# Performance work log

Hardware: AMD Instinct MI355X
Metric: run time of the kernel (lower is better)

Reference implementation:

```python
import jax, jax.numpy as jnp
import numpy as np

N = 12288   # nodes
E = 393216  # edges (avg degree 32)
B = 16      # graphs in batch
F_IN = 15   # node feature dim
H = 32      # hidden_dim
EMB = 64    # embedding_dim
NC = 11     # num_classes
EDIM = 2    # edge feature dim
EPS = 1e-5  # BatchNorm eps


def _bn(x, gamma, beta):
    # training-mode BatchNorm1d: biased batch variance, matches torch normalization
    mu = jnp.mean(x, axis=0)
    var = jnp.var(x, axis=0)
    return gamma * (x - mu) * jax.lax.rsqrt(var + EPS) + beta


def setup_inputs() -> dict:
    key = jax.random.key(0)
    ks = jax.random.split(key, 16)
    def p(k, shape, s=0.05):
        return jax.random.normal(k, shape, dtype=jnp.float32) * s
    z = lambda *s: jnp.zeros(s, jnp.float32)
    o = lambda *s: jnp.ones(s, jnp.float32)
    return {
        "x": jax.random.normal(ks[0], (N, F_IN), dtype=jnp.float32),
        "edge_attr": jax.random.normal(ks[1], (E, EDIM), dtype=jnp.float32),
        "w_edge": p(ks[2], (EDIM, 1)), "b_edge": z(1),
        "w1": p(ks[3], (F_IN, H)), "b1": z(H), "g1": o(H), "be1": z(H),
        "w2": p(ks[4], (H, 2 * H)), "b2": z(2 * H), "g2": o(2 * H), "be2": z(2 * H),
        "w3": p(ks[5], (2 * H, EMB)), "b3": z(EMB), "g3": o(EMB), "be3": z(EMB),
        "wf1": p(ks[6], (EMB, 512)), "bf1": z(512), "gf1": o(512), "bef1": z(512),
        "wf2": p(ks[7], (512, 256)), "bf2": z(256), "gf2": o(256), "bef2": z(256),
        "wf3": p(ks[8], (256, NC)), "bf3": z(NC),
        "edge_index": jax.random.randint(ks[9], (2, E), 0, N, dtype=jnp.int64)
                      if jax.config.jax_enable_x64 else jax.random.randint(ks[9], (2, E), 0, N),
        "batch": jnp.sort(jax.random.randint(ks[10], (N,), 0, B)),
    }


def reference(x, edge_attr, w_edge, b_edge,
              w1, b1, g1, be1, w2, b2, g2, be2, w3, b3, g3, be3,
              wf1, bf1, gf1, bef1, wf2, bf2, gf2, bef2, wf3, bf3,
              edge_index, batch):
    # edge weights: sigmoid(Linear(edge_attr)) -> [E]
    ew = jax.nn.sigmoid(edge_attr @ w_edge + b_edge)[:, 0]
    # dense adjacency with self loops, accumulate duplicates (sparse_coo.to_dense)
    loop = jnp.arange(N)
    row = jnp.concatenate([edge_index[0], loop])
    col = jnp.concatenate([edge_index[1], loop])
    w_aug = jnp.concatenate([ew, jnp.ones((N,), ew.dtype)])
    adj = jnp.zeros((N, N), ew.dtype).at[row, col].add(w_aug)
    # symmetric degree normalization D^-1/2 A D^-1/2
    deg = adj.sum(axis=1)
    dis = jnp.where(deg > 0, jax.lax.rsqrt(jnp.where(deg > 0, deg, 1.0)), 0.0)
    support = dis[:, None] * adj * dis[None, :]
    # three GCN layers: support @ x @ W + b, BN, relu
    h = jax.nn.relu(_bn(support @ x @ w1 + b1, g1, be1))
    h = jax.nn.relu(_bn(support @ h @ w2 + b2, g2, be2))
    h = jax.nn.relu(_bn(support @ h @ w3 + b3, g3, be3))
    # global max pool per graph (empty graphs -> zeros)
    seg = jax.ops.segment_max(h, batch, num_segments=B)
    cnt = jax.ops.segment_sum(jnp.ones((N,), h.dtype), batch, num_segments=B)
    emb = jnp.where(cnt[:, None] > 0, seg, 0.0)
    # MLP head (dropout = identity at inference)
    o = jax.nn.relu(_bn(emb @ wf1 + bf1, gf1, bef1))
    o = jax.nn.relu(_bn(o @ wf2 + bf2, gf2, bef2))
    logits = o @ wf3 + bf3
    return jax.nn.log_softmax(logits, axis=1), emb
```

## Files before the change

### kernel.cpp

```cpp
#include <hip/hip_runtime.h>

#define NN   12288
#define EE   393216
#define WELL 128
#define NELL (NN*WELL)
#define BG   16
#define FIN  15
#define FH1  32
#define FH2  64
#define NCL  11
#define BNEPS 1e-5f
#define NBANK 32

typedef unsigned long long u64;
static inline int cdiv(long a, long b){ return (int)((a + b - 1) / b); }

__device__ __forceinline__ int getIdx(const void* p, long i, int is64){
  return is64 ? (int)((const long long*)p)[i] : ((const int*)p)[i];
}

__device__ __forceinline__ float degOf(unsigned lo){
  return 1.0f + (float)lo * (1.0f/1048576.0f);
}

__global__ void k_pre(u64* deg_cnt, float* csp1, float* csp2, float* csp3,
                      float* embf, float* xp, const float* x,
                      const void* ei, const void* batch, int* flags){
  int g = blockIdx.x*256 + threadIdx.x;
  if (g < NN){
    deg_cnt[g] = 0ull;
    float v[16];
    #pragma unroll
    for (int j = 0; j < 15; j++) v[j] = x[g*15 + j];
    v[15] = 0.f;
    float4* dst = (float4*)(xp + g*16);
    dst[0] = make_float4(v[0],  v[1],  v[2],  v[3]);
    dst[1] = make_float4(v[4],  v[5],  v[6],  v[7]);
    dst[2] = make_float4(v[8],  v[9],  v[10], v[11]);
    dst[3] = make_float4(v[12], v[13], v[14], v[15]);
  }
  if (g < NBANK*128){ csp1[g] = 0.f; csp2[g] = 0.f; csp3[g] = 0.f; }
  if (g < BG*64) embf[g] = 0.f;
  if (blockIdx.x == 0 && threadIdx.x < 64){
    const int* a = (const int*)ei;
    unsigned long long m0 = __ballot(a[2*threadIdx.x + 1] == 0);
    const int* b = (const int*)batch;
    int j = 96*threadIdx.x;
    unsigned long long m1 = __ballot(b[2*j + 1] == 0);
    if (threadIdx.x == 0){
      flags[0] = (m0 == ~0ull) ? 1 : 0;
      flags[1] = (m1 == ~0ull) ? 1 : 0;
    }
  }
}

__global__ void k_edge(const float* ea, const float* we, const float* bedg,
                       const void* ei, const int* flags, u64* deg_cnt,
                       unsigned* csr_p){
  int e = blockIdx.x*256 + threadIdx.x;
  if (e >= EE) return;
  int is64 = flags[0];
  float2 eav = ((const float2*)ea)[e];
  float z = eav.x*we[0] + eav.y*we[1] + bedg[0];
  float w = 1.0f/(1.0f + expf(-z));
  int r = getIdx(ei, e, is64);
  int c = getIdx(ei, (long)EE + e, is64);
  u64 add = (1ull << 32) | (u64)__float2uint_rn(w * 1048576.0f);
  u64 old = atomicAdd(&deg_cnt[r], add);
  int slot = (int)(old >> 32);
  if (slot < WELL){
    unsigned wfix = __float2uint_rn(w * 131072.0f);
    csr_p[((long)r << 7) + slot] = (unsigned)c | (wfix << 14);
  }
}

__global__ void __launch_bounds__(256) k_fix2(const u64* __restrict__ deg_cnt,
                                              unsigned* __restrict__ csr_p){
  int row = blockIdx.x*4 + (threadIdx.x >> 6);
  int lane = threadIdx.x & 63;
  const unsigned* cl = (const unsigned*)deg_cnt;
  int n = (int)(deg_cnt[row] >> 32);
  n = n < WELL ? n : WELL;
  for (int s = lane; s < n; s += 64){
    long idx = ((long)row << 7) + s;
    unsigned v = csr_p[idx];
    int c = (int)(v & 16383u);
    float w = (float)(v >> 14) * (1.0f/131072.0f);
    w *= rsqrtf(degOf(cl[2*c]));
    csr_p[idx] = (unsigned)c | (__float2uint_rn(w * 131072.0f) << 14);
  }
}

template<int F, int FUSE, int LPR, int KS, int FO, int APPLY_BN>
__global__ void __launch_bounds__(256) k_layerv(
    const float* __restrict__ Hin,
    const float* __restrict__ cspin, const float* __restrict__ gam,
    const float* __restrict__ bet,
    const float* __restrict__ W, const float* __restrict__ bias,
    const u64* __restrict__ deg_cnt, const unsigned* __restrict__ csr_p,
    float* __restrict__ Pout, float* __restrict__ csout){
  const int R = 256/(LPR*KS);
  __shared__ __align__(16) float At[R][F];
  __shared__ float4 Apart[256];
  __shared__ float lcs[FO], lcq[FO];
  __shared__ float lsc[64], lsh[64];
  int tid = threadIdx.x;
  if (tid < FO){ lcs[tid] = 0.f; lcq[tid] = 0.f; }
  if (APPLY_BN && tid < F){
    float s = 0.f, q = 0.f;
    #pragma unroll
    for (int b = 0; b < NBANK; b++){
      s += cspin[b*128 + tid];
      q += cspin[b*128 + 64 + tid];
    }
    float mu  = s*(1.0f/NN);
    float var = q*(1.0f/NN) - mu*mu;
    float sc = gam[tid]*rsqrtf(var + BNEPS);
    lsc[tid] = sc;
    lsh[tid] = bet[tid] - mu*sc;
  }
  __syncthreads();
  int fl = tid % LPR;
  int sub = tid / LPR;
  int kw = sub % KS, lr = sub / KS;
  int f0 = fl*4;
  float sc0 = 1.f, sc1 = 1.f, sc2 = 1.f, sc3 = 1.f;
  float sh0 = 0.f, sh1 = 0.f, sh2 = 0.f, sh3 = 0.f;
  if (APPLY_BN){
    sc0 = lsc[f0]; sc1 = lsc[f0+1]; sc2 = lsc[f0+2]; sc3 = lsc[f0+3];
    sh0 = lsh[f0]; sh1 = lsh[f0+1]; sh2 = lsh[f0+2]; sh3 = lsh[f0+3];
  }
  int row = blockIdx.x*R + lr;
  u64 dc = deg_cnt[row];
  float d = rsqrtf(degOf((unsigned)(dc & 0xffffffffull)));
  int n = (int)(dc >> 32);
  n = n < WELL ? n : WELL;
  const float4* __restrict__ Hin4 = (const float4*)Hin;
  float ax = 0.f, ay = 0.f, az = 0.f, aw = 0.f;
  if (kw == 0){
    float4 v = Hin4[row*LPR + fl];
    if (APPLY_BN){
      ax = d * fmaxf(v.x*sc0 + sh0, 0.f);
      ay = d * fmaxf(v.y*sc1 + sh1, 0.f);
      az = d * fmaxf(v.z*sc2 + sh2, 0.f);
      aw = d * fmaxf(v.w*sc3 + sh3, 0.f);
    } else {
      ax = d*v.x; ay = d*v.y; az = d*v.z; aw = d*v.w;
    }
  }
  int nch = (n + 7) >> 3;
  const uint4* pb = (const uint4*)(csr_p + ((long)row << 7));
  int ch = kw;
  if (ch < nch){
    uint4 q0 = pb[2*ch], q1 = pb[2*ch+1];
    while (true){
      int chn = ch + KS;
      bool more = (chn < nch);
      uint4 p0, p1;
      if (more){ p0 = pb[2*chn]; p1 = pb[2*chn+1]; }
      unsigned pv[8];
      pv[0]=q0.x; pv[1]=q0.y; pv[2]=q0.z; pv[3]=q0.w;
      pv[4]=q1.x; pv[5]=q1.y; pv[6]=q1.z; pv[7]=q1.w;
      int base = ch*8;
      if (base + 8 > n){
        #pragma unroll
        for (int j = 0; j < 8; j++) if (base + j >= n) pv[j] = 0u;
      }
      float4 h4[8];
      #pragma unroll
      for (int j = 0; j < 8; j++)
        h4[j] = Hin4[(int)(pv[j] & 16383u)*LPR + fl];
      #pragma unroll
      for (int j = 0; j < 8; j++){
        float w = (float)(pv[j] >> 14) * (1.0f/131072.0f);
        float hx = h4[j].x, hy = h4[j].y, hz = h4[j].z, hw = h4[j].w;
        if (APPLY_BN){
          hx = fmaxf(hx*sc0 + sh0, 0.f);
          hy = fmaxf(hy*sc1 + sh1, 0.f);
          hz = fmaxf(hz*sc2 + sh2, 0.f);
          hw = fmaxf(hw*sc3 + sh3, 0.f);
        }
        ax += w*hx; ay += w*hy; az += w*hz; aw += w*hw;
      }
      if (!more) break;
      ch = chn; q0 = p0; q1 = p1;
    }
  }
  Apart[tid] = make_float4(ax, ay, az, aw);
  __syncthreads();
  if (kw == 0){
    #pragma unroll
    for (int k = 1; k < KS; k++){
      float4 p = Apart[tid + k*LPR];
      ax += p.x; ay += p.y; az += p.z; aw += p.w;
    }
    float4* atrow = (float4*)&At[lr][0];
    atrow[fl] = make_float4(d*ax, d*ay, d*az, d*aw);
  }
  __syncthreads();
  const int fo = tid % FO;
  float bb = bias[fo];
  for (int o = tid; o < R*FO; o += 256){
    int l = o / FO;
    float s = bb;
    const float4* at4 = (const float4*)&At[l][0];
    #pragma unroll
    for (int fi4 = 0; fi4 < FUSE/4; fi4++){
      float4 a = at4[fi4];
      s += a.x * W[(fi4*4 + 0)*FO + fo];
      s += a.y * W[(fi4*4 + 1)*FO + fo];
      s += a.z * W[(fi4*4 + 2)*FO + fo];
      s += a.w * W[(fi4*4 + 3)*FO + fo];
    }
    #pragma unroll
    for (int fi = (FUSE/4)*4; fi < FUSE; fi++)
      s += At[l][fi] * W[fi*FO + fo];
    Pout[(blockIdx.x*R + l)*FO + fo] = s;
    atomicAdd(&lcs[fo], s);
    atomicAdd(&lcq[fo], s*s);
  }
  __syncthreads();
  if (tid < FO){
    int bank = blockIdx.x & (NBANK-1);
    atomicAdd(&csout[bank*128 + tid],      lcs[tid]);
    atomicAdd(&csout[bank*128 + 64 + tid], lcq[tid]);
  }
}

__global__ void k_pool(const float* P3, const float* csp, const float* gam,
                       const float* bet, const void* batch, const int* flags,
                       float* embf){
  __shared__ float lsc[64], lsh[64];
  if (threadIdx.x < 64){
    float s = 0.f, q = 0.f;
    #pragma unroll
    for (int b = 0; b < NBANK; b++){
      s += csp[b*128 + threadIdx.x];
      q += csp[b*128 + 64 + threadIdx.x];
    }
    float mu  = s*(1.0f/NN);
    float var = q*(1.0f/NN) - mu*mu;
    float sc = gam[threadIdx.x]*rsqrtf(var + BNEPS);
    lsc[threadIdx.x] = sc;
    lsh[threadIdx.x] = bet[threadIdx.x] - mu*sc;
  }
  __syncthreads();
  int is64 = flags[1];
  int b = blockIdx.x & 15, chunk = blockIdx.x >> 4;
  int lo = 0, hi = NN;
  while (lo < hi){ int m = (lo+hi)>>1; if (getIdx(batch, m, is64) < b) lo = m+1; else hi = m; }
  int start = lo;
  lo = start; hi = NN;
  while (lo < hi){ int m = (lo+hi)>>1; if (getIdx(batch, m, is64) < b+1) lo = m+1; else hi = m; }
  int end = lo;
  int f = threadIdx.x & 63, grp = threadIdx.x >> 6;
  float sc = lsc[f], sh = lsh[f];
  float m = 0.0f;
  for (int i = start + chunk*4 + grp; i < end; i += 64)
    m = fmaxf(m, P3[(long)i*FH2 + f]*sc + sh);
  __shared__ float shm[4][64];
  shm[grp][f] = m;
  __syncthreads();
  if (grp == 0){
    float v = fmaxf(fmaxf(shm[0][f], shm[1][f]), fmaxf(shm[2][f], shm[3][f]));
    atomicMax((int*)&embf[b*64 + f], __float_as_int(v));
  }
}

__global__ void __launch_bounds__(256) k_fcA(const float* embf, const float* wf1,
    const float* bf1, const float* gf1, const float* bef1, float* s1g, float* out){
  if (blockIdx.x == 0){
    #pragma unroll
    for (int i = 0; i < 4; i++)
      out[BG*NCL + i*256 + threadIdx.x] = embf[i*256 + threadIdx.x];
  }
  int c = blockIdx.x*4 + (threadIdx.x >> 6);
  int l = threadIdx.x & 63;
  float wcol = wf1[l*512 + c];
  float z[BG];
  #pragma unroll
  for (int r = 0; r < BG; r++){
    float v = embf[r*64 + l] * wcol;
    #pragma unroll
    for (int off = 32; off > 0; off >>= 1) v += __shfl_down(v, off);
    z[r] = v;
  }
  if (l == 0){
    float bb = bf1[c];
    float s = 0.f, q = 0.f;
    #pragma unroll
    for (int r = 0; r < BG; r++){ float zr = z[r] + bb; s += zr; q += zr*zr; }
    float mean = s*(1.f/BG), var = q*(1.f/BG) - mean*mean;
    float inv = rsqrtf(var + BNEPS);
    float gg = gf1[c], b2 = bef1[c];
    #pragma unroll
    for (int r = 0; r < BG; r++)
      s1g[r*512 + c] = fmaxf(gg*(z[r] + bb - mean)*inv + b2, 0.f);
  }
}

__global__ void __launch_bounds__(256) k_fcB(const float* s1g, const float* wf2,
    const float* bf2, const float* gf2, const float* bef2, float* s2g){
  int c = blockIdx.x*4 + (threadIdx.x >> 6);
  int l = threadIdx.x & 63;
  float wreg[8];
  #pragma unroll
  for (int j = 0; j < 8; j++) wreg[j] = wf2[(l + 64*j)*256 + c];
  float z[BG];
  #pragma unroll
  for (int r = 0; r < BG; r++){
    float v = 0.f;
    #pragma unroll
    for (int j = 0; j < 8; j++) v += s1g[r*512 + l + 64*j] * wreg[j];
    #pragma unroll
    for (int off = 32; off > 0; off >>= 1) v += __shfl_down(v, off);
    z[r] = v;
  }
  if (l == 0){
    float bb = bf2[c];
    float s = 0.f, q = 0.f;
    #pragma unroll
    for (int r = 0; r < BG; r++){ float zr = z[r] + bb; s += zr; q += zr*zr; }
    float mean = s*(1.f/BG), var = q*(1.f/BG) - mean*mean;
    float inv = rsqrtf(var + BNEPS);
    float gg = gf2[c], b2 = bef2[c];
    #pragma unroll
    for (int r = 0; r < BG; r++)
      s2g[r*256 + c] = fmaxf(gg*(z[r] + bb - mean)*inv + b2, 0.f);
  }
}

__global__ void k_fc3(const float* s2g, const float* wf3, const float* bf3, float* out){
  __shared__ float s2[BG*256];
  __shared__ float sl[BG*NCL];
  int t = threadIdx.x;
  for (int i = t; i < BG*256; i += 256) s2[i] = s2g[i];
  __syncthreads();
  if (t < BG*NCL){
    int r = t / NCL, c = t - r*NCL;
    float s = bf3[c];
    for (int k = 0; k < 256; k++) s += s2[r*256 + k]*wf3[k*NCL + c];
    sl[t] = s;
  }
  __syncthreads();
  if (t < BG){
    float m = -1e30f;
    for (int c = 0; c < NCL; c++) m = fmaxf(m, sl[t*NCL + c]);
    float s = 0.f;
    for (int c = 0; c < NCL; c++) s += expf(sl[t*NCL + c] - m);
    float lg = logf(s) + m;
    for (int c = 0; c < NCL; c++) out[t*NCL + c] = sl[t*NCL + c] - lg;
  }
}

extern "C" void kernel_launch(void* const* d_in, const int* in_sizes, int n_in,
                              void* d_out, int out_size, void* d_ws, size_t ws_size,
                              hipStream_t stream){
  const float* x    = (const float*)d_in[0];
  const float* ea   = (const float*)d_in[1];
  const float* we   = (const float*)d_in[2];
  const float* bedg = (const float*)d_in[3];
  const float* w1   = (const float*)d_in[4];  const float* b1  = (const float*)d_in[5];
  const float* g1   = (const float*)d_in[6];  const float* be1 = (const float*)d_in[7];
  const float* w2   = (const float*)d_in[8];  const float* b2  = (const float*)d_in[9];
  const float* g2   = (const float*)d_in[10]; const float* be2 = (const float*)d_in[11];
  const float* w3   = (const float*)d_in[12]; const float* b3  = (const float*)d_in[13];
  const float* g3   = (const float*)d_in[14]; const float* be3 = (const float*)d_in[15];
  const float* wf1  = (const float*)d_in[16]; const float* bf1 = (const float*)d_in[17];
  const float* gf1  = (const float*)d_in[18]; const float* bef1= (const float*)d_in[19];
  const float* wf2  = (const float*)d_in[20]; const float* bf2 = (const float*)d_in[21];
  const float* gf2  = (const float*)d_in[22]; const float* bef2= (const float*)d_in[23];
  const float* wf3  = (const float*)d_in[24]; const float* bf3 = (const float*)d_in[25];
  const void* ei    = d_in[26];
  const void* batch = d_in[27];
  float* out = (float*)d_out;

  u64* wq = (u64*)d_ws;
  u64* deg_cnt = wq; wq += NN;
  unsigned* csr_p = (unsigned*)wq; wq += NELL/2;
  float* ws = (float*)wq;
  float* xp    = ws; ws += NN*16;
  float* P1    = ws; ws += NN*FH1;
  float* P2    = ws; ws += NN*FH2;
  float* P3    = ws; ws += NN*FH2;
  float* csp1  = ws; ws += NBANK*128;
  float* csp2  = ws; ws += NBANK*128;
  float* csp3  = ws; ws += NBANK*128;
  float* embf  = ws; ws += BG*64;
  float* s1g   = ws; ws += BG*512;
  float* s2g   = ws; ws += BG*256;
  int* flags   = (int*)ws;

  k_pre<<<48, 256, 0, stream>>>(deg_cnt, csp1, csp2, csp3, embf, xp, x,
                                ei, batch, flags);
  k_edge<<<cdiv(EE,256), 256, 0, stream>>>(ea, we, bedg, ei, flags, deg_cnt, csr_p);
  k_fix2<<<NN/4, 256, 0, stream>>>(deg_cnt, csr_p);

  k_layerv<16,FIN,4,8,FH1,0><<<NN/8, 256, 0, stream>>>(xp,
      nullptr, nullptr, nullptr, w1, b1, deg_cnt, csr_p, P1, csp1);
  k_layerv<FH1,FH1,8,4,FH2,1><<<NN/8, 256, 0, stream>>>(P1, csp1, g1, be1,
      w2, b2, deg_cnt, csr_p, P2, csp2);
  k_layerv<FH2,FH2,16,4,FH2,1><<<NN/4, 256, 0, stream>>>(P2, csp2, g2, be2,
      w3, b3, deg_cnt, csr_p, P3, csp3);

  k_pool<<<256, 256, 0, stream>>>(P3, csp3, g3, be3, batch, flags, embf);
  k_fcA<<<128, 256, 0, stream>>>(embf, wf1, bf1, gf1, bef1, s1g, out);
  k_fcB<<<64, 256, 0, stream>>>(s1g, wf2, bf2, gf2, bef2, s2g);
  k_fc3<<<1, 256, 0, stream>>>(s2g, wf3, bf3, out);
}
```

Baseline: 223.4 us.

## Store intermediate GCN layer activations in fp16 to halve gather traffic

Layers 1 and 2 now write their pre-BN outputs as half precision. A new k_layerh kernel gathers 8 halves per 16-byte load, converts them to float, and applies BN and ReLU before accumulating in fp32. This halves the bytes moved by the random neighbor gathers in layers 2 and 3 and changes the lane and row mapping and the grid size for layer 3. In exchange it rounds the activations to fp16, which reduces accuracy, and adds conversion instructions.

```diff
diff --git a/kernel.cpp b/kernel.cpp
--- a/kernel.cpp
+++ b/kernel.cpp
@@ -1,4 +1,5 @@
 #include <hip/hip_runtime.h>
+#include <hip/hip_fp16.h>
 
 #define NN   12288
 #define EE   393216
@@ -91,45 +92,22 @@
   }
 }
 
-template<int F, int FUSE, int LPR, int KS, int FO, int APPLY_BN>
+template<int F, int FUSE, int LPR, int KS, int FO>
 __global__ void __launch_bounds__(256) k_layerv(
     const float* __restrict__ Hin,
-    const float* __restrict__ cspin, const float* __restrict__ gam,
-    const float* __restrict__ bet,
     const float* __restrict__ W, const float* __restrict__ bias,
     const u64* __restrict__ deg_cnt, const unsigned* __restrict__ csr_p,
-    float* __restrict__ Pout, float* __restrict__ csout){
+    __half* __restrict__ Pout, float* __restrict__ csout){
   const int R = 256/(LPR*KS);
   __shared__ __align__(16) float At[R][F];
   __shared__ float4 Apart[256];
   __shared__ float lcs[FO], lcq[FO];
-  __shared__ float lsc[64], lsh[64];
   int tid = threadIdx.x;
   if (tid < FO){ lcs[tid] = 0.f; lcq[tid] = 0.f; }
-  if (APPLY_BN && tid < F){
-    float s = 0.f, q = 0.f;
-    #pragma unroll
-    for (int b = 0; b < NBANK; b++){
-      s += cspin[b*128 + tid];
-      q += cspin[b*128 + 64 + tid];
-    }
-    float mu  = s*(1.0f/NN);
-    float var = q*(1.0f/NN) - mu*mu;
-    float sc = gam[tid]*rsqrtf(var + BNEPS);
-    lsc[tid] = sc;
-    lsh[tid] = bet[tid] - mu*sc;
-  }
   __syncthreads();
   int fl = tid % LPR;
   int sub = tid / LPR;
   int kw = sub % KS, lr = sub / KS;
-  int f0 = fl*4;
-  float sc0 = 1.f, sc1 = 1.f, sc2 = 1.f, sc3 = 1.f;
-  float sh0 = 0.f, sh1 = 0.f, sh2 = 0.f, sh3 = 0.f;
-  if (APPLY_BN){
-    sc0 = lsc[f0]; sc1 = lsc[f0+1]; sc2 = lsc[f0+2]; sc3 = lsc[f0+3];
-    sh0 = lsh[f0]; sh1 = lsh[f0+1]; sh2 = lsh[f0+2]; sh3 = lsh[f0+3];
-  }
   int row = blockIdx.x*R + lr;
   u64 dc = deg_cnt[row];
   float d = rsqrtf(degOf((unsigned)(dc & 0xffffffffull)));
@@ -139,14 +117,7 @@
   float ax = 0.f, ay = 0.f, az = 0.f, aw = 0.f;
   if (kw == 0){
     float4 v = Hin4[row*LPR + fl];
-    if (APPLY_BN){
-      ax = d * fmaxf(v.x*sc0 + sh0, 0.f);
-      ay = d * fmaxf(v.y*sc1 + sh1, 0.f);
-      az = d * fmaxf(v.z*sc2 + sh2, 0.f);
-      aw = d * fmaxf(v.w*sc3 + sh3, 0.f);
-    } else {
-      ax = d*v.x; ay = d*v.y; az = d*v.z; aw = d*v.w;
-    }
+    ax = d*v.x; ay = d*v.y; az = d*v.z; aw = d*v.w;
   }
   int nch = (n + 7) >> 3;
   const uint4* pb = (const uint4*)(csr_p + ((long)row << 7));
@@ -173,14 +144,7 @@
       #pragma unroll
       for (int j = 0; j < 8; j++){
         float w = (float)(pv[j] >> 14) * (1.0f/131072.0f);
-        float hx = h4[j].x, hy = h4[j].y, hz = h4[j].z, hw = h4[j].w;
-        if (APPLY_BN){
-          hx = fmaxf(hx*sc0 + sh0, 0.f);
-          hy = fmaxf(hy*sc1 + sh1, 0.f);
-          hz = fmaxf(hz*sc2 + sh2, 0.f);
-          hw = fmaxf(hw*sc3 + sh3, 0.f);
-        }
-        ax += w*hx; ay += w*hy; az += w*hz; aw += w*hw;
+        ax += w*h4[j].x; ay += w*h4[j].y; az += w*h4[j].z; aw += w*h4[j].w;
       }
       if (!more) break;
       ch = chn; q0 = p0; q1 = p1;
@@ -215,7 +179,140 @@
     #pragma unroll
     for (int fi = (FUSE/4)*4; fi < FUSE; fi++)
       s += At[l][fi] * W[fi*FO + fo];
-    Pout[(blockIdx.x*R + l)*FO + fo] = s;
+    Pout[(blockIdx.x*R + l)*FO + fo] = __float2half(s);
+    atomicAdd(&lcs[fo], s);
+    atomicAdd(&lcq[fo], s*s);
+  }
+  __syncthreads();
+  if (tid < FO){
+    int bank = blockIdx.x & (NBANK-1);
+    atomicAdd(&csout[bank*128 + tid],      lcs[tid]);
+    atomicAdd(&csout[bank*128 + 64 + tid], lcq[tid]);
+  }
+}
+
+template<int F, int LPR, int KS, int FO, int OUTH>
+__global__ void __launch_bounds__(256) k_layerh(
+    const __half* __restrict__ Hin,
+    const float* __restrict__ cspin, const float* __restrict__ gam,
+    const float* __restrict__ bet,
+    const float* __restrict__ W, const float* __restrict__ bias,
+    const u64* __restrict__ deg_cnt, const unsigned* __restrict__ csr_p,
+    void* __restrict__ PoutV, float* __restrict__ csout){
+  const int R = 256/(LPR*KS);
+  __shared__ __align__(16) float At[R][F];
+  __shared__ float Apart[256][8];
+  __shared__ float lcs[FO], lcq[FO];
+  __shared__ float lsc[64], lsh[64];
+  int tid = threadIdx.x;
+  if (tid < FO){ lcs[tid] = 0.f; lcq[tid] = 0.f; }
+  if (tid < F){
+    float s = 0.f, q = 0.f;
+    #pragma unroll
+    for (int b = 0; b < NBANK; b++){
+      s += cspin[b*128 + tid];
+      q += cspin[b*128 + 64 + tid];
+    }
+    float mu  = s*(1.0f/NN);
+    float var = q*(1.0f/NN) - mu*mu;
+    float sc = gam[tid]*rsqrtf(var + BNEPS);
+    lsc[tid] = sc;
+    lsh[tid] = bet[tid] - mu*sc;
+  }
+  __syncthreads();
+  int fl = tid % LPR;
+  int sub = tid / LPR;
+  int kw = sub % KS, lr = sub / KS;
+  int f0 = fl*8;
+  float scv[8], shv[8];
+  #pragma unroll
+  for (int k = 0; k < 8; k++){ scv[k] = lsc[f0+k]; shv[k] = lsh[f0+k]; }
+  int row = blockIdx.x*R + lr;
+  u64 dc = deg_cnt[row];
+  float d = rsqrtf(degOf((unsigned)(dc & 0xffffffffull)));
+  int n = (int)(dc >> 32);
+  n = n < WELL ? n : WELL;
+  const float4* __restrict__ Hin4 = (const float4*)Hin;
+  float ax[8];
+  #pragma unroll
+  for (int k = 0; k < 8; k++) ax[k] = 0.f;
+  if (kw == 0){
+    float4 raw = Hin4[row*LPR + fl];
+    const __half2* hp = (const __half2*)&raw;
+    float2 u0 = __half22float2(hp[0]), u1 = __half22float2(hp[1]);
+    float2 u2 = __half22float2(hp[2]), u3 = __half22float2(hp[3]);
+    float hv[8] = {u0.x,u0.y,u1.x,u1.y,u2.x,u2.y,u3.x,u3.y};
+    #pragma unroll
+    for (int k = 0; k < 8; k++)
+      ax[k] = d * fmaxf(hv[k]*scv[k] + shv[k], 0.f);
+  }
+  int nch = (n + 7) >> 3;
+  const uint4* pb = (const uint4*)(csr_p + ((long)row << 7));
+  int ch = kw;
+  if (ch < nch){
+    uint4 q0 = pb[2*ch], q1 = pb[2*ch+1];
+    while (true){
+      int chn = ch + KS;
+      bool more = (chn < nch);
+      uint4 p0, p1;
+      if (more){ p0 = pb[2*chn]; p1 = pb[2*chn+1]; }
+      unsigned pv[8];
+      pv[0]=q0.x; pv[1]=q0.y; pv[2]=q0.z; pv[3]=q0.w;
+      pv[4]=q1.x; pv[5]=q1.y; pv[6]=q1.z; pv[7]=q1.w;
+      int base = ch*8;
+      if (base + 8 > n){
+        #pragma unroll
+        for (int j = 0; j < 8; j++) if (base + j >= n) pv[j] = 0u;
+      }
+      float4 g4[8];
+      #pragma unroll
+      for (int j = 0; j < 8; j++)
+        g4[j] = Hin4[(int)(pv[j] & 16383u)*LPR + fl];
+      #pragma unroll
+      for (int j = 0; j < 8; j++){
+        float w = (float)(pv[j] >> 14) * (1.0f/131072.0f);
+        const __half2* hp = (const __half2*)&g4[j];
+        float2 u0 = __half22float2(hp[0]), u1 = __half22float2(hp[1]);
+        float2 u2 = __half22float2(hp[2]), u3 = __half22float2(hp[3]);
+        float hv[8] = {u0.x,u0.y,u1.x,u1.y,u2.x,u2.y,u3.x,u3.y};
+        #pragma unroll
+        for (int k = 0; k < 8; k++)
+          ax[k] += w * fmaxf(hv[k]*scv[k] + shv[k], 0.f);
+      }
+      if (!more) break;
+      ch = chn; q0 = p0; q1 = p1;
+    }
+  }
+  #pragma unroll
+  for (int k = 0; k < 8; k++) Apart[tid][k] = ax[k];
+  __syncthreads();
+  if (kw == 0){
+    #pragma unroll
+    for (int ks = 1; ks < KS; ks++){
+      #pragma unroll
+      for (int k = 0; k < 8; k++) ax[k] += Apart[tid + ks*LPR][k];
+    }
+    float4* atrow = (float4*)&At[lr][f0];
+    atrow[0] = make_float4(d*ax[0], d*ax[1], d*ax[2], d*ax[3]);
+    atrow[1] = make_float4(d*ax[4], d*ax[5], d*ax[6], d*ax[7]);
+  }
+  __syncthreads();
+  const int fo = tid % FO;
+  float bb = bias[fo];
+  for (int o = tid; o < R*FO; o += 256){
+    int l = o / FO;
+    float s = bb;
+    const float4* at4 = (const float4*)&At[l][0];
+    #pragma unroll
+    for (int fi4 = 0; fi4 < F/4; fi4++){
+      float4 a = at4[fi4];
+      s += a.x * W[(fi4*4 + 0)*FO + fo];
+      s += a.y * W[(fi4*4 + 1)*FO + fo];
+      s += a.z * W[(fi4*4 + 2)*FO + fo];
+      s += a.w * W[(fi4*4 + 3)*FO + fo];
+    }
+    if (OUTH) ((__half*)PoutV)[(blockIdx.x*R + l)*FO + fo] = __float2half(s);
+    else      ((float*)PoutV)[(blockIdx.x*R + l)*FO + fo] = s;
     atomicAdd(&lcs[fo], s);
     atomicAdd(&lcq[fo], s*s);
   }
@@ -380,8 +477,8 @@
   unsigned* csr_p = (unsigned*)wq; wq += NELL/2;
   float* ws = (float*)wq;
   float* xp    = ws; ws += NN*16;
-  float* P1    = ws; ws += NN*FH1;
-  float* P2    = ws; ws += NN*FH2;
+  __half* P1h  = (__half*)ws; ws += NN*FH1/2;
+  __half* P2h  = (__half*)ws; ws += NN*FH2/2;
   float* P3    = ws; ws += NN*FH2;
   float* csp1  = ws; ws += NBANK*128;
   float* csp2  = ws; ws += NBANK*128;
@@ -396,12 +493,12 @@
   k_edge<<<cdiv(EE,256), 256, 0, stream>>>(ea, we, bedg, ei, flags, deg_cnt, csr_p);
   k_fix2<<<NN/4, 256, 0, stream>>>(deg_cnt, csr_p);
 
-  k_layerv<16,FIN,4,8,FH1,0><<<NN/8, 256, 0, stream>>>(xp,
-      nullptr, nullptr, nullptr, w1, b1, deg_cnt, csr_p, P1, csp1);
-  k_layerv<FH1,FH1,8,4,FH2,1><<<NN/8, 256, 0, stream>>>(P1, csp1, g1, be1,
-      w2, b2, deg_cnt, csr_p, P2, csp2);
-  k_layerv<FH2,FH2,16,4,FH2,1><<<NN/4, 256, 0, stream>>>(P2, csp2, g2, be2,
-      w3, b3, deg_cnt, csr_p, P3, csp3);
+  k_layerv<16,FIN,4,8,FH1><<<NN/8, 256, 0, stream>>>(xp,
+      w1, b1, deg_cnt, csr_p, P1h, csp1);
+  k_layerh<FH1,4,8,FH2,1><<<NN/8, 256, 0, stream>>>(P1h, csp1, g1, be1,
+      w2, b2, deg_cnt, csr_p, (void*)P2h, csp2);
+  k_layerh<FH2,8,4,FH2,0><<<NN/8, 256, 0, stream>>>(P2h, csp2, g2, be2,
+      w3, b3, deg_cnt, csr_p, (void*)P3, csp3);
 
   k_pool<<<256, 256, 0, stream>>>(P3, csp3, g3, be3, batch, flags, embf);
   k_fcA<<<128, 256, 0, stream>>>(embf, wf1, bf1, gf1, bef1, s1g, out);
```

Result: no change. 222.3 us (-0.5%).
